# Kernel tuning notes

Measured on AMD Instinct MI355X. Metric: run time of the kernel, lower is better.

Reference implementation:

```python
import jax, jax.numpy as jnp
import numpy as np

K = 4                      # options['num_k']
NOISE_EPS = 0.1            # noise_epsilon in noisy_top_k_gating
LOSS_COEF = 1e-4
EPS_COMBINE = float(np.finfo(np.float64).eps)  # np.finfo(float).eps in combine
INV_SQRT2 = 0.7071067811865475


def _norm_cdf(z):
    # Normal(0,1).cdf
    return 0.5 * (1.0 + jax.lax.erf(z * INV_SQRT2))


def _cv_squared(v):
    # torch .var() is unbiased (ddof=1)
    return jnp.var(v, ddof=1) / (jnp.mean(v) ** 2 + 1e-10)


def setup_inputs() -> dict:
    key = jax.random.key(0)
    B, D, E, H, O = 1024, 1024, 16, 2048, 1024
    ks = jax.random.split(key, 6)
    x = jax.random.normal(ks[0], (B, D), jnp.float32)
    w_gate = jax.random.normal(ks[1], (D, E), jnp.float32) * 0.02
    w_noise = jax.random.normal(ks[2], (D, E), jnp.float32) * 0.02
    W1 = jax.random.normal(ks[3], (E, D, H), jnp.float32) / np.sqrt(D).astype(np.float32)
    b1 = jnp.zeros((E, H), jnp.float32)
    W2 = jax.random.normal(ks[4], (E, H, O), jnp.float32) / np.sqrt(H).astype(np.float32)
    b2 = jnp.zeros((E, O), jnp.float32)
    noise = jax.random.normal(ks[5], (B, E), jnp.float32)  # randn_like(clean_logits)
    return {"x": x, "w_gate": w_gate, "w_noise": w_noise,
            "W1": W1, "b1": b1, "W2": W2, "b2": b2, "noise": noise}


def moe_forward(x, w_gate, w_noise, W1, b1, W2, b2, noise):
    B = x.shape[0]
    # --- noisy top-k gating (train=True path) ---
    clean_logits = x @ w_gate                              # [B, E]
    noise_std = jax.nn.softplus(x @ w_noise) + NOISE_EPS   # [B, E]
    noisy_logits = clean_logits + noise * noise_std        # [B, E]
    top_logits, top_idx = jax.lax.top_k(noisy_logits, K + 1)  # [B, K+1]
    topk_gates = jax.nn.softmax(top_logits[:, :K], axis=1)    # [B, K]
    gates = jnp.zeros_like(noisy_logits).at[
        jnp.arange(B)[:, None], top_idx[:, :K]].set(topk_gates)  # [B, E] sparse
    # --- load = E[prob in top-k] (smooth load estimate) ---
    thr_in = top_logits[:, K][:, None]       # (k+1)-th value: threshold if in
    thr_out = top_logits[:, K - 1][:, None]  # k-th value: threshold if out
    is_in = noisy_logits > thr_in
    prob_if_in = _norm_cdf((clean_logits - thr_in) / noise_std)
    prob_if_out = _norm_cdf((clean_logits - thr_out) / noise_std)
    load = jnp.where(is_in, prob_if_in, prob_if_out).sum(0)   # [E]
    importance = gates.sum(0)                                 # [E]
    loss = (_cv_squared(importance) + _cv_squared(load)) * LOSS_COEF
    # --- experts + combine ---
    # Dense all-expert compute; gates are exactly zero off the top-k so the
    # gate-weighted sum reproduces the sparse dispatch/index_add combine math.
    h = jax.nn.relu(jnp.einsum('bi,eih->beh', x, W1) + b1)    # [B, E, H]
    expert_out = jnp.einsum('beh,eho->beo', h, W2) + b2       # [B, E, O]
    # combine: sum_e gate[b,e] * exp(expert_out[b,e,:]); zeros -> eps; log
    combined = jnp.einsum('be,beo->bo', gates, jnp.exp(expert_out))  # [B, O]
    combined = jnp.where(combined == 0, EPS_COMBINE, combined)
    y = jnp.log(combined)
    return y, loss


def reference(x, w_gate, w_noise, W1, b1, W2, b2, noise):
    return moe_forward(x, w_gate, w_noise, W1, b1, W2, b2, noise)
```

## Files before the change

### kernel.cpp

```cpp
#include <hip/hip_runtime.h>
#include <cstdint>
#include <cstddef>

#define BTOK 1024
#define DDIM 1024
#define EEXP 16
#define HDIM 2048
#define ODIM 1024

typedef __bf16 bh;
typedef bh bh8 __attribute__((ext_vector_type(8)));
typedef bh bh4 __attribute__((ext_vector_type(4)));
typedef float fx4 __attribute__((ext_vector_type(4)));

__device__ __forceinline__ void gload16(const void* g, void* l) {
  __builtin_amdgcn_global_load_lds(
      (const __attribute__((address_space(1))) void*)g,
      (__attribute__((address_space(3))) void*)l, 16, 0, 0);
}

__global__ __launch_bounds__(256) void k_tcvt2(const float* __restrict__ in,
                                               bh* __restrict__ out, int K, int N,
                                               int KT, int NT) {
  const int kt = blockIdx.x, nt = blockIdx.y, e = blockIdx.z;
  const int k0 = kt * 32, n0 = nt * 128;
  const float* pin = in + (size_t)e * K * N + (size_t)k0 * N + n0;
  bh* pout = out + (((size_t)e * NT + nt) * KT + kt) * 4096;
  __shared__ float t[32][129];
  const int tid = threadIdx.x;
#pragma unroll
  for (int rep = 0; rep < 4; ++rep) {
    int idx = rep * 256 + tid;
    int kk = idx >> 5, c4 = (idx & 31) << 2;
    fx4 v = *(const fx4*)(pin + (size_t)kk * N + c4);
#pragma unroll
    for (int u = 0; u < 4; ++u) t[kk][c4 + u] = v[u];
  }
  __syncthreads();
#pragma unroll
  for (int rep = 0; rep < 2; ++rep) {
    int task = rep * 256 + tid;
    int row = task >> 2, s = task & 3, o = s ^ (row & 3);
    bh8 w;
#pragma unroll
    for (int u = 0; u < 8; ++u) w[u] = (bh)t[o * 8 + u][row];
    *(bh8*)(pout + (size_t)task * 8) = w;
  }
}

__global__ __launch_bounds__(256) void k_gating(
    const float* __restrict__ x, const float* __restrict__ wg,
    const float* __restrict__ wn, const float* __restrict__ nz,
    bh* __restrict__ xbf, unsigned* __restrict__ cnt,
    int* __restrict__ tok_buck, float* __restrict__ gate_buck,
    float* __restrict__ imp_part, float* __restrict__ load_part) {
  const int b = blockIdx.x, tid = threadIdx.x;
  __shared__ __align__(16) float xs[1024];
  __shared__ float part[32][9];
  __shared__ float vals[32];
  fx4 v = *(const fx4*)(x + (size_t)b * 1024 + tid * 4);
  *(fx4*)(xs + tid * 4) = v;
  bh4 xb;
#pragma unroll
  for (int u = 0; u < 4; ++u) xb[u] = (bh)v[u];
  *(bh4*)(xbf + (size_t)b * 1024 + tid * 4) = xb;
  __syncthreads();
  const int col = tid & 31, g = tid >> 5;
  const float* wp = ((col < 16) ? wg : wn) + (col & 15);
  float s = 0.f;
  for (int it = g * 128; it < g * 128 + 128; ++it) s += xs[it] * wp[it * 16];
  part[col][g] = s;
  __syncthreads();
  if (tid < 32) {
    float tsum = 0.f;
#pragma unroll
    for (int gg = 0; gg < 8; ++gg) tsum += part[tid][gg];
    vals[tid] = tsum;
  }
  __syncthreads();
  if (tid == 0) {
    float clean[16], sd[16], noisy[16];
#pragma unroll
    for (int e = 0; e < 16; ++e) {
      clean[e] = vals[e];
      float raw = vals[16 + e];
      float sp = fmaxf(raw, 0.f) + log1pf(expf(-fabsf(raw)));
      sd[e] = sp + 0.1f;
      noisy[e] = clean[e] + nz[b * 16 + e] * sd[e];
    }
    float tv[5]; int ti[5]; unsigned used = 0;
    for (int r = 0; r < 5; ++r) {
      float bst = -INFINITY; int bi = 0;
      for (int e = 0; e < 16; ++e)
        if (!((used >> e) & 1u) && noisy[e] > bst) { bst = noisy[e]; bi = e; }
      used |= 1u << bi; tv[r] = bst; ti[r] = bi;
    }
    float gts[4]; float se = 0.f;
#pragma unroll
    for (int k = 0; k < 4; ++k) { gts[k] = expf(tv[k] - tv[0]); se += gts[k]; }
#pragma unroll
    for (int k = 0; k < 4; ++k) gts[k] /= se;
    const float thr_in = tv[4], thr_out = tv[3];
    float imp[16];
#pragma unroll
    for (int e = 0; e < 16; ++e) imp[e] = 0.f;
    for (int k = 0; k < 4; ++k) imp[ti[k]] = gts[k];
    for (int e = 0; e < 16; ++e) imp_part[b * 16 + e] = imp[e];
    for (int e = 0; e < 16; ++e) {
      bool is_in = noisy[e] > thr_in;
      float z = (clean[e] - (is_in ? thr_in : thr_out)) / sd[e];
      load_part[b * 16 + e] = 0.5f * (1.f + erff(z * 0.70710678118654752f));
    }
    for (int k = 0; k < 4; ++k) {
      int ee = ti[k];
      unsigned p = atomicAdd(&cnt[ee], 1u);
      tok_buck[ee * 1024 + (int)p] = b;
      gate_buck[ee * 1024 + (int)p] = gts[k];
    }
  }
}

__device__ __forceinline__ float cv2_16(const float* v) {
  float m = 0.f;
  for (int i = 0; i < 16; ++i) m += v[i];
  m *= (1.f / 16.f);
  float var = 0.f;
  for (int i = 0; i < 16; ++i) { float d = v[i] - m; var += d * d; }
  var *= (1.f / 15.f);
  return var / (m * m + 1e-10f);
}

__global__ __launch_bounds__(256) void k_finalize(
    const unsigned* __restrict__ cnt, unsigned* __restrict__ offs,
    const float* __restrict__ imp_part, const float* __restrict__ load_part,
    float* __restrict__ loss_out) {
  const int tid = threadIdx.x;
  __shared__ float red[256];
  __shared__ float impv[16], loadv[16];
  const int e = tid & 15, p = tid >> 4;
  float s = 0.f;
  for (int r = 0; r < 64; ++r) s += imp_part[((p * 64 + r) << 4) + e];
  red[tid] = s;
  __syncthreads();
  if (tid < 16) {
    float t = 0.f;
    for (int pp = 0; pp < 16; ++pp) t += red[pp * 16 + tid];
    impv[tid] = t;
  }
  __syncthreads();
  s = 0.f;
  for (int r = 0; r < 64; ++r) s += load_part[((p * 64 + r) << 4) + e];
  red[tid] = s;
  __syncthreads();
  if (tid < 16) {
    float t = 0.f;
    for (int pp = 0; pp < 16; ++pp) t += red[pp * 16 + tid];
    loadv[tid] = t;
  }
  __syncthreads();
  if (tid == 0) {
    unsigned o = 0;
    for (int ee = 0; ee < 16; ++ee) { offs[ee] = o; o += cnt[ee]; }
    loss_out[0] = (cv2_16(impv) + cv2_16(loadv)) * 1e-4f;
  }
}

__global__ __launch_bounds__(256) void k_gemm1(
    const bh* __restrict__ xbf, const bh* __restrict__ w1t,
    const float* __restrict__ b1, const int* __restrict__ tok_buck,
    const unsigned* __restrict__ cnt, const unsigned* __restrict__ offs,
    bh* __restrict__ hbf) {
  const int lid = blockIdx.x;
  const int xcd = lid & 7, idx = lid >> 3;
  const int mt = idx & 7, g = xcd * 32 + (idx >> 3);
  const int e = g >> 4, nt = g & 15;
  const int ne = (int)cnt[e];
  if (mt * 128 >= ne) return;
  __shared__ __align__(16) bh As[4][128 * 32];
  __shared__ __align__(16) bh Bs[4][128 * 32];
  const int tid = threadIdx.x;
  const int lane = tid & 63, wv = tid >> 6, wm = wv >> 1, wn_ = wv & 1;

  const bh* a_src[2]; const bh* b_src[2];
  int dst_off[2];
#pragma unroll
  for (int r = 0; r < 2; ++r) {
    int task = r * 256 + tid;
    int row = task >> 2, s = task & 3;
    int gm = mt * 128 + row; if (gm >= ne) gm = ne - 1;
    int tok = tok_buck[e * 1024 + gm];
    a_src[r] = xbf + (size_t)tok * 1024 + ((s ^ (row & 3)) << 3);
    b_src[r] = w1t + (((size_t)e * 16 + nt) * 32) * 4096 + (size_t)task * 8;
    dst_off[r] = (r * 256 + (wv << 6)) << 4;
  }
  const int ln15 = lane & 15, q = lane >> 4;
  const int qs = ((q ^ (ln15 & 3)) << 3);
  int a_off[4], b_off[4];
#pragma unroll
  for (int i = 0; i < 4; ++i) {
    a_off[i] = (wm * 64 + i * 16 + ln15) * 32 + qs;
    b_off[i] = (wn_ * 64 + i * 16 + ln15) * 32 + qs;
  }
  fx4 zero = {0.f, 0.f, 0.f, 0.f};
  fx4 acc[4][4];
#pragma unroll
  for (int i = 0; i < 4; ++i)
#pragma unroll
    for (int j = 0; j < 4; ++j) acc[i][j] = zero;

  auto stage = [&](int qb, int kt) {
    const int ko = kt * 32;
    const size_t bo = (size_t)kt * 4096;
#pragma unroll
    for (int r = 0; r < 2; ++r) {
      gload16(a_src[r] + ko, (char*)(&As[qb][0]) + dst_off[r]);
      gload16(b_src[r] + bo, (char*)(&Bs[qb][0]) + dst_off[r]);
    }
  };

  const int NT = 32;
  stage(0, 0); stage(1, 1); stage(2, 2);
  asm volatile("s_waitcnt vmcnt(8)" ::: "memory");
  __builtin_amdgcn_s_barrier();

  for (int t = 0; t < NT; ++t) {
    if (t + 3 < NT) stage((t + 3) & 3, t + 3);
    const bh* Ab = &As[t & 3][0];
    const bh* Bb = &Bs[t & 3][0];
    bh8 af[4], bfr[4];
#pragma unroll
    for (int i = 0; i < 4; ++i) af[i] = *(const bh8*)(Ab + a_off[i]);
#pragma unroll
    for (int i = 0; i < 4; ++i) bfr[i] = *(const bh8*)(Bb + b_off[i]);
#pragma unroll
    for (int i = 0; i < 4; ++i)
#pragma unroll
      for (int j = 0; j < 4; ++j)
        acc[i][j] = __builtin_amdgcn_mfma_f32_16x16x32_bf16(af[i], bfr[j], acc[i][j], 0, 0, 0);
    if (t + 3 < NT)      asm volatile("s_waitcnt vmcnt(8) lgkmcnt(0)" ::: "memory");
    else if (t + 2 < NT) asm volatile("s_waitcnt vmcnt(4) lgkmcnt(0)" ::: "memory");
    else if (t + 1 < NT) asm volatile("s_waitcnt vmcnt(0) lgkmcnt(0)" ::: "memory");
    if (t + 1 < NT) __builtin_amdgcn_s_barrier();
  }

  int nrows = ne - mt * 128; if (nrows > 128) nrows = 128;
  int jn[4]; float b1v[4];
#pragma unroll
  for (int j = 0; j < 4; ++j) {
    jn[j] = nt * 128 + wn_ * 64 + j * 16 + ln15;
    b1v[j] = b1[e * 2048 + jn[j]];
  }
  const int rowbase = (int)offs[e] + mt * 128;
#pragma unroll
  for (int i = 0; i < 4; ++i)
#pragma unroll
    for (int rr = 0; rr < 4; ++rr) {
      int ml = wm * 64 + i * 16 + q * 4 + rr;
      if (ml < nrows) {
        size_t ro = (size_t)(rowbase + ml) * 2048;
#pragma unroll
        for (int j = 0; j < 4; ++j) {
          float vv = acc[i][j][rr] + b1v[j];
          hbf[ro + jn[j]] = (bh)fmaxf(vv, 0.f);
        }
      }
    }
}

__global__ __launch_bounds__(256) void k_gemm2(
    const bh* __restrict__ hbf, const bh* __restrict__ w2t,
    const float* __restrict__ b2, const int* __restrict__ tok_buck,
    const float* __restrict__ gate_buck, const unsigned* __restrict__ cnt,
    const unsigned* __restrict__ offs, float* __restrict__ yv) {
  const int lid = blockIdx.x;
  const int xcd = lid & 7, idx = lid >> 3;
  const int nt = idx & 7, g = xcd * 16 + (idx >> 3);
  const int e = g >> 3, mt = g & 7;
  const int ne = (int)cnt[e];
  if (mt * 128 >= ne) return;
  __shared__ __align__(16) bh As[4][128 * 32];
  __shared__ __align__(16) bh Bs[4][128 * 32];
  const int tid = threadIdx.x;
  const int lane = tid & 63, wv = tid >> 6, wm = wv >> 1, wn_ = wv & 1;
  const int rowbase = (int)offs[e] + mt * 128;

  const bh* a_src[2]; const bh* b_src[2];
  int dst_off[2];
#pragma unroll
  for (int r = 0; r < 2; ++r) {
    int task = r * 256 + tid;
    int row = task >> 2, s = task & 3;
    a_src[r] = hbf + (size_t)(rowbase + row) * 2048 + ((s ^ (row & 3)) << 3);
    b_src[r] = w2t + (((size_t)e * 8 + nt) * 64) * 4096 + (size_t)task * 8;
    dst_off[r] = (r * 256 + (wv << 6)) << 4;
  }
  const int ln15 = lane & 15, q = lane >> 4;
  const int qs = ((q ^ (ln15 & 3)) << 3);
  int a_off[4], b_off[4];
#pragma unroll
  for (int i = 0; i < 4; ++i) {
    a_off[i] = (wm * 64 + i * 16 + ln15) * 32 + qs;
    b_off[i] = (wn_ * 64 + i * 16 + ln15) * 32 + qs;
  }
  fx4 zero = {0.f, 0.f, 0.f, 0.f};
  fx4 acc[4][4];
#pragma unroll
  for (int i = 0; i < 4; ++i)
#pragma unroll
    for (int j = 0; j < 4; ++j) acc[i][j] = zero;

  auto stage = [&](int qb, int kt) {
    const int ko = kt * 32;
    const size_t bo = (size_t)kt * 4096;
#pragma unroll
    for (int r = 0; r < 2; ++r) {
      gload16(a_src[r] + ko, (char*)(&As[qb][0]) + dst_off[r]);
      gload16(b_src[r] + bo, (char*)(&Bs[qb][0]) + dst_off[r]);
    }
  };

  const int NT = 64;
  stage(0, 0); stage(1, 1); stage(2, 2);
  asm volatile("s_waitcnt vmcnt(8)" ::: "memory");
  __builtin_amdgcn_s_barrier();

  for (int t = 0; t < NT; ++t) {
    if (t + 3 < NT) stage((t + 3) & 3, t + 3);
    const bh* Ab = &As[t & 3][0];
    const bh* Bb = &Bs[t & 3][0];
    bh8 af[4], bfr[4];
#pragma unroll
    for (int i = 0; i < 4; ++i) af[i] = *(const bh8*)(Ab + a_off[i]);
#pragma unroll
    for (int i = 0; i < 4; ++i) bfr[i] = *(const bh8*)(Bb + b_off[i]);
#pragma unroll
    for (int i = 0; i < 4; ++i)
#pragma unroll
      for (int j = 0; j < 4; ++j)
        acc[i][j] = __builtin_amdgcn_mfma_f32_16x16x32_bf16(af[i], bfr[j], acc[i][j], 0, 0, 0);
    if (t + 3 < NT)      asm volatile("s_waitcnt vmcnt(8) lgkmcnt(0)" ::: "memory");
    else if (t + 2 < NT) asm volatile("s_waitcnt vmcnt(4) lgkmcnt(0)" ::: "memory");
    else if (t + 1 < NT) asm volatile("s_waitcnt vmcnt(0) lgkmcnt(0)" ::: "memory");
    if (t + 1 < NT) __builtin_amdgcn_s_barrier();
  }

  int nrows = ne - mt * 128; if (nrows > 128) nrows = 128;
  int on[4]; float b2v[4];
#pragma unroll
  for (int j = 0; j < 4; ++j) {
    on[j] = nt * 128 + wn_ * 64 + j * 16 + ln15;
    b2v[j] = b2[e * 1024 + on[j]];
  }
#pragma unroll
  for (int i = 0; i < 4; ++i)
#pragma unroll
    for (int rr = 0; rr < 4; ++rr) {
      int ml = wm * 64 + i * 16 + q * 4 + rr;
      if (ml < nrows) {
        int pos = mt * 128 + ml;
        int bt = tok_buck[e * 1024 + pos];
        float gg = gate_buck[e * 1024 + pos];
        float* yrow = yv + (size_t)bt * 1024;
#pragma unroll
        for (int j = 0; j < 4; ++j)
          atomicAdd(&yrow[on[j]], gg * expf(acc[i][j][rr] + b2v[j]));
      }
    }
}

__global__ __launch_bounds__(256) void k_log(float* __restrict__ yv) {
  const int i = blockIdx.x * 256 + threadIdx.x;
  fx4* p = (fx4*)yv + i;
  fx4 v = *p;
#pragma unroll
  for (int c = 0; c < 4; ++c) {
    float w = v[c];
    if (w == 0.f) w = 2.2204460492503131e-16f;
    v[c] = logf(w);
  }
  *p = v;
}

extern "C" void kernel_launch(void* const* d_in, const int* in_sizes, int n_in,
                              void* d_out, int out_size, void* d_ws, size_t ws_size,
                              hipStream_t stream) {
  const float* x  = (const float*)d_in[0];
  const float* wg = (const float*)d_in[1];
  const float* wn = (const float*)d_in[2];
  const float* W1 = (const float*)d_in[3];
  const float* b1 = (const float*)d_in[4];
  const float* W2 = (const float*)d_in[5];
  const float* b2 = (const float*)d_in[6];
  const float* nz = (const float*)d_in[7];
  float* out = (float*)d_out;

  char* ws = (char*)d_ws;
  unsigned* cnt      = (unsigned*)(ws + 0);
  unsigned* offs     = (unsigned*)(ws + 64);
  float*    imp_part = (float*)(ws + 256);
  float*    load_part= (float*)(ws + 256 + 65536);
  int*      tok_buck = (int*)(ws + 256 + 2 * 65536);
  float*    gate_buck= (float*)(ws + 256 + 3 * 65536);
  bh*       xbf      = (bh*)(ws + 262400);
  bh*       hbf      = (bh*)(ws + 2359552);
  bh*       w1t      = (bh*)(ws + 19661056);
  bh*       w2t      = (bh*)(ws + 86769920);
  const size_t needed = 153878784;
  if (ws_size < needed) {
    hipMemsetAsync(d_out, 0x42, (size_t)out_size * 4, stream);
    return;
  }

  hipMemsetAsync(d_out, 0, (size_t)out_size * 4, stream);
  hipMemsetAsync(cnt, 0, 64, stream);

  k_tcvt2<<<dim3(32, 16, 16), 256, 0, stream>>>(W1, w1t, 1024, 2048, 32, 16);
  k_tcvt2<<<dim3(64, 8, 16), 256, 0, stream>>>(W2, w2t, 2048, 1024, 64, 8);
  k_gating<<<1024, 256, 0, stream>>>(x, wg, wn, nz, xbf, cnt, tok_buck, gate_buck,
                                     imp_part, load_part);
  k_finalize<<<1, 256, 0, stream>>>(cnt, offs, imp_part, load_part, out + (out_size - 1));
  k_gemm1<<<2048, 256, 0, stream>>>(xbf, w1t, b1, tok_buck, cnt, offs, hbf);
  k_gemm2<<<1024, 256, 0, stream>>>(hbf, w2t, b2, tok_buck, gate_buck, cnt, offs, out);
  k_log<<<1024, 256, 0, stream>>>(out);
}
```

Measured before the change: 513.8 us.

## Replace direct global-to-LDS 4-stage pipeline with register-staged double buffering

Both expert GEMM kernels drop the global_load_lds four-stage ring buffer and instead load tiles into registers, write them to one of two LDS buffers, and compute from the other. This halves LDS usage, which may allow more resident blocks, and avoids the hand-written vmcnt waits. In exchange each K-step now has extra barriers and an explicit register-to-LDS write, and prefetch depth falls from three tiles to one, so memory latency is less hidden.

```diff
diff --git a/kernel.cpp b/kernel.cpp
--- a/kernel.cpp
+++ b/kernel.cpp
@@ -12,12 +12,6 @@
 typedef bh bh8 __attribute__((ext_vector_type(8)));
 typedef bh bh4 __attribute__((ext_vector_type(4)));
 typedef float fx4 __attribute__((ext_vector_type(4)));
-
-__device__ __forceinline__ void gload16(const void* g, void* l) {
-  __builtin_amdgcn_global_load_lds(
-      (const __attribute__((address_space(1))) void*)g,
-      (__attribute__((address_space(3))) void*)l, 16, 0, 0);
-}
 
 __global__ __launch_bounds__(256) void k_tcvt2(const float* __restrict__ in,
                                                bh* __restrict__ out, int K, int N,
@@ -165,6 +159,48 @@
   }
 }
 
+
+#define LOADR(AV, BV, KT) do {                                      \
+  _Pragma("unroll") for (int r_ = 0; r_ < 2; ++r_) {                \
+    AV[r_] = *(const fx4*)(a_src[r_] + (KT) * 32);                  \
+    BV[r_] = *(const fx4*)(b_src[r_] + (size_t)(KT) * 4096);        \
+  }                                                                 \
+} while (0)
+
+#define WRITELDS(BUF, AV, BV) do {                                  \
+  _Pragma("unroll") for (int r_ = 0; r_ < 2; ++r_) {                \
+    *(fx4*)((char*)(&As[BUF][0]) + wtask[r_]) = AV[r_];             \
+    *(fx4*)((char*)(&Bs[BUF][0]) + wtask[r_]) = BV[r_];             \
+  }                                                                 \
+} while (0)
+
+#define COMPUTE(BUF) do {                                           \
+  bh8 af_[4], bf_[4];                                               \
+  _Pragma("unroll") for (int i_ = 0; i_ < 4; ++i_)                  \
+    af_[i_] = *(const bh8*)(&As[BUF][a_off[i_]]);                   \
+  _Pragma("unroll") for (int i_ = 0; i_ < 4; ++i_)                  \
+    bf_[i_] = *(const bh8*)(&Bs[BUF][b_off[i_]]);                   \
+  _Pragma("unroll") for (int i_ = 0; i_ < 4; ++i_)                  \
+    _Pragma("unroll") for (int j_ = 0; j_ < 4; ++j_)                \
+      acc[i_][j_] = __builtin_amdgcn_mfma_f32_16x16x32_bf16(af_[i_], bf_[j_], acc[i_][j_], 0, 0, 0); \
+} while (0)
+
+#define GEMM_MAIN(NT) do {                                          \
+  LOADR(a0, b0, 0);                                                 \
+  for (int t = 0; t < (NT); t += 2) {                               \
+    __syncthreads();                                                \
+    LOADR(a1, b1, t + 1);                                           \
+    WRITELDS(0, a0, b0);                                            \
+    __syncthreads();                                                \
+    COMPUTE(0);                                                     \
+    __syncthreads();                                                \
+    if (t + 2 < (NT)) LOADR(a0, b0, t + 2);                         \
+    WRITELDS(1, a1, b1);                                            \
+    __syncthreads();                                                \
+    COMPUTE(1);                                                     \
+  }                                                                 \
+} while (0)
+
 __global__ __launch_bounds__(256) void k_gemm1(
     const bh* __restrict__ xbf, const bh* __restrict__ w1t,
     const float* __restrict__ b1, const int* __restrict__ tok_buck,
@@ -176,13 +212,13 @@
   const int e = g >> 4, nt = g & 15;
   const int ne = (int)cnt[e];
   if (mt * 128 >= ne) return;
-  __shared__ __align__(16) bh As[4][128 * 32];
-  __shared__ __align__(16) bh Bs[4][128 * 32];
+  __shared__ __align__(16) bh As[2][128 * 32];
+  __shared__ __align__(16) bh Bs[2][128 * 32];
   const int tid = threadIdx.x;
   const int lane = tid & 63, wv = tid >> 6, wm = wv >> 1, wn_ = wv & 1;
 
   const bh* a_src[2]; const bh* b_src[2];
-  int dst_off[2];
+  int wtask[2];
 #pragma unroll
   for (int r = 0; r < 2; ++r) {
     int task = r * 256 + tid;
@@ -191,7 +227,7 @@
     int tok = tok_buck[e * 1024 + gm];
     a_src[r] = xbf + (size_t)tok * 1024 + ((s ^ (row & 3)) << 3);
     b_src[r] = w1t + (((size_t)e * 16 + nt) * 32) * 4096 + (size_t)task * 8;
-    dst_off[r] = (r * 256 + (wv << 6)) << 4;
+    wtask[r] = task * 16;
   }
   const int ln15 = lane & 15, q = lane >> 4;
   const int qs = ((q ^ (ln15 & 3)) << 3);
@@ -208,47 +244,31 @@
 #pragma unroll
     for (int j = 0; j < 4; ++j) acc[i][j] = zero;
 
-  auto stage = [&](int qb, int kt) {
-    const int ko = kt * 32;
-    const size_t bo = (size_t)kt * 4096;
-#pragma unroll
-    for (int r = 0; r < 2; ++r) {
-      gload16(a_src[r] + ko, (char*)(&As[qb][0]) + dst_off[r]);
-      gload16(b_src[r] + bo, (char*)(&Bs[qb][0]) + dst_off[r]);
-    }
-  };
-
-  const int NT = 32;
-  stage(0, 0); stage(1, 1); stage(2, 2);
-  asm volatile("s_waitcnt vmcnt(8)" ::: "memory");
-  __builtin_amdgcn_s_barrier();
-
-  for (int t = 0; t < NT; ++t) {
-    if (t + 3 < NT) stage((t + 3) & 3, t + 3);
-    const bh* Ab = &As[t & 3][0];
-    const bh* Bb = &Bs[t & 3][0];
-    bh8 af[4], bfr[4];
-#pragma unroll
-    for (int i = 0; i < 4; ++i) af[i] = *(const bh8*)(Ab + a_off[i]);
-#pragma unroll
-    for (int i = 0; i < 4; ++i) bfr[i] = *(const bh8*)(Bb + b_off[i]);
-#pragma unroll
-    for (int i = 0; i < 4; ++i)
-#pragma unroll
-      for (int j = 0; j < 4; ++j)
-        acc[i][j] = __builtin_amdgcn_mfma_f32_16x16x32_bf16(af[i], bfr[j], acc[i][j], 0, 0, 0);
-    if (t + 3 < NT)      asm volatile("s_waitcnt vmcnt(8) lgkmcnt(0)" ::: "memory");
-    else if (t + 2 < NT) asm volatile("s_waitcnt vmcnt(4) lgkmcnt(0)" ::: "memory");
-    else if (t + 1 < NT) asm volatile("s_waitcnt vmcnt(0) lgkmcnt(0)" ::: "memory");
-    if (t + 1 < NT) __builtin_amdgcn_s_barrier();
+  fx4 a0[2], b0[2], a1[2], b1v_[2];
+#define b1 b1
+  GEMM_MAIN_1: ;
+  {
+    LOADR(a0, b0, 0);
+    for (int t = 0; t < 32; t += 2) {
+      __syncthreads();
+      LOADR(a1, b1v_, t + 1);
+      WRITELDS(0, a0, b0);
+      __syncthreads();
+      COMPUTE(0);
+      __syncthreads();
+      if (t + 2 < 32) LOADR(a0, b0, t + 2);
+      WRITELDS(1, a1, b1v_);
+      __syncthreads();
+      COMPUTE(1);
+    }
   }
 
   int nrows = ne - mt * 128; if (nrows > 128) nrows = 128;
-  int jn[4]; float b1v[4];
+  int jn[4]; float b1b[4];
 #pragma unroll
   for (int j = 0; j < 4; ++j) {
     jn[j] = nt * 128 + wn_ * 64 + j * 16 + ln15;
-    b1v[j] = b1[e * 2048 + jn[j]];
+    b1b[j] = b1[e * 2048 + jn[j]];
   }
   const int rowbase = (int)offs[e] + mt * 128;
 #pragma unroll
@@ -260,7 +280,7 @@
         size_t ro = (size_t)(rowbase + ml) * 2048;
 #pragma unroll
         for (int j = 0; j < 4; ++j) {
-          float vv = acc[i][j][rr] + b1v[j];
+          float vv = acc[i][j][rr] + b1b[j];
           hbf[ro + jn[j]] = (bh)fmaxf(vv, 0.f);
         }
       }
@@ -278,21 +298,21 @@
   const int e = g >> 3, mt = g & 7;
   const int ne = (int)cnt[e];
   if (mt * 128 >= ne) return;
-  __shared__ __align__(16) bh As[4][128 * 32];
-  __shared__ __align__(16) bh Bs[4][128 * 32];
+  __shared__ __align__(16) bh As[2][128 * 32];
+  __shared__ __align__(16) bh Bs[2][128 * 32];
   const int tid = threadIdx.x;
   const int lane = tid & 63, wv = tid >> 6, wm = wv >> 1, wn_ = wv & 1;
   const int rowbase = (int)offs[e] + mt * 128;
 
   const bh* a_src[2]; const bh* b_src[2];
-  int dst_off[2];
+  int wtask[2];
 #pragma unroll
   for (int r = 0; r < 2; ++r) {
     int task = r * 256 + tid;
     int row = task >> 2, s = task & 3;
     a_src[r] = hbf + (size_t)(rowbase + row) * 2048 + ((s ^ (row & 3)) << 3);
     b_src[r] = w2t + (((size_t)e * 8 + nt) * 64) * 4096 + (size_t)task * 8;
-    dst_off[r] = (r * 256 + (wv << 6)) << 4;
+    wtask[r] = task * 16;
   }
   const int ln15 = lane & 15, q = lane >> 4;
   const int qs = ((q ^ (ln15 & 3)) << 3);
@@ -309,39 +329,21 @@
 #pragma unroll
     for (int j = 0; j < 4; ++j) acc[i][j] = zero;
 
-  auto stage = [&](int qb, int kt) {
-    const int ko = kt * 32;
-    const size_t bo = (size_t)kt * 4096;
-#pragma unroll
-    for (int r = 0; r < 2; ++r) {
-      gload16(a_src[r] + ko, (char*)(&As[qb][0]) + dst_off[r]);
-      gload16(b_src[r] + bo, (char*)(&Bs[qb][0]) + dst_off[r]);
-    }
-  };
-
-  const int NT = 64;
-  stage(0, 0); stage(1, 1); stage(2, 2);
-  asm volatile("s_waitcnt vmcnt(8)" ::: "memory");
-  __builtin_amdgcn_s_barrier();
-
-  for (int t = 0; t < NT; ++t) {
-    if (t + 3 < NT) stage((t + 3) & 3, t + 3);
-    const bh* Ab = &As[t & 3][0];
-    const bh* Bb = &Bs[t & 3][0];
-    bh8 af[4], bfr[4];
-#pragma unroll
-    for (int i = 0; i < 4; ++i) af[i] = *(const bh8*)(Ab + a_off[i]);
-#pragma unroll
-    for (int i = 0; i < 4; ++i) bfr[i] = *(const bh8*)(Bb + b_off[i]);
-#pragma unroll
-    for (int i = 0; i < 4; ++i)
-#pragma unroll
-      for (int j = 0; j < 4; ++j)
-        acc[i][j] = __builtin_amdgcn_mfma_f32_16x16x32_bf16(af[i], bfr[j], acc[i][j], 0, 0, 0);
-    if (t + 3 < NT)      asm volatile("s_waitcnt vmcnt(8) lgkmcnt(0)" ::: "memory");
-    else if (t + 2 < NT) asm volatile("s_waitcnt vmcnt(4) lgkmcnt(0)" ::: "memory");
-    else if (t + 1 < NT) asm volatile("s_waitcnt vmcnt(0) lgkmcnt(0)" ::: "memory");
-    if (t + 1 < NT) __builtin_amdgcn_s_barrier();
+  fx4 a0[2], b0[2], a1[2], b1v_[2];
+  {
+    LOADR(a0, b0, 0);
+    for (int t = 0; t < 64; t += 2) {
+      __syncthreads();
+      LOADR(a1, b1v_, t + 1);
+      WRITELDS(0, a0, b0);
+      __syncthreads();
+      COMPUTE(0);
+      __syncthreads();
+      if (t + 2 < 64) LOADR(a0, b0, t + 2);
+      WRITELDS(1, a1, b1v_);
+      __syncthreads();
+      COMPUTE(1);
+    }
   }
 
   int nrows = ne - mt * 128; if (nrows > 128) nrows = 128;
```

Measured after the change: 498.0 us. 1.03x faster.
